# Kernel tuning notes

Measured on AMD Instinct MI355X. Metric: run time of the kernel, lower is better.

Reference implementation:

```python
import jax, jax.numpy as jnp
import numpy as np

B, T, C, H = 8, 2048, 1024, 128

def setup_inputs() -> dict:
    key = jax.random.key(0)
    k1, k2, k3, k4 = jax.random.split(key, 4)
    x = jax.random.normal(k1, (B, T, C), dtype=jnp.float32)
    Wq = jax.random.normal(k2, (C, H), dtype=jnp.float32) * (C ** -0.5)
    Wk = jax.random.normal(k3, (C, H), dtype=jnp.float32) * (C ** -0.5)
    Wv = jax.random.normal(k4, (C, H), dtype=jnp.float32) * (C ** -0.5)
    return {"x": x, "Wq": Wq, "Wk": Wk, "Wv": Wv}

def reference(x, Wq, Wk, Wv):
    # x: [B,T,C]; projections (no bias)
    q = jnp.einsum('btc,ch->bth', x, Wq)
    k = jnp.einsum('btc,ch->bth', x, Wk)
    v = jnp.einsum('btc,ch->bth', x, Wv)
    # NOTE: original module has NO 1/sqrt(head_size) scaling
    scores = jnp.einsum('bth,bsh->bts', q, k)  # [B,T,T]
    t = scores.shape[1]
    causal = jnp.tril(jnp.ones((t, t), dtype=bool))
    scores = jnp.where(causal, scores, -jnp.inf)
    attn = jax.nn.softmax(scores, axis=-1)  # dropout is identity in eval
    out = jnp.einsum('bts,bsh->bth', attn, v)  # [B,T,H]
    return out
```

## Files before the change

kernel.cpp:

```cpp
#include <hip/hip_runtime.h>

typedef __bf16 bf16;
typedef _Float16 f16;
typedef f16 f16x4 __attribute__((ext_vector_type(4)));
typedef f16 f16x8 __attribute__((ext_vector_type(8)));
typedef float f32x4 __attribute__((ext_vector_type(4)));

#define MFMA_FP(a, b, c) __builtin_amdgcn_mfma_f32_16x16x32_f16((a), (b), (c), 0, 0, 0)

static constexpr int Bn = 8, T = 2048, C = 1024, H = 128;
static constexpr int M = Bn * T;

__device__ __forceinline__ void gll16(const void* g, void* l) {
  __builtin_amdgcn_global_load_lds(
      (const __attribute__((address_space(1))) unsigned int*)g,
      (__attribute__((address_space(3))) unsigned int*)l, 16, 0, 0);
}

__global__ __launch_bounds__(256) void kwt(const float* __restrict__ Wq,
                                           const float* __restrict__ Wk,
                                           const float* __restrict__ Wv,
                                           f16* __restrict__ wt) {
  __shared__ float tl[32][33];
  const int w = blockIdx.z;
  const float* src = (w == 0) ? Wq : (w == 1) ? Wk : Wv;
  f16* dh = wt + (size_t)w * H * C;
  const int k0 = blockIdx.x * 32, n0 = blockIdx.y * 32;
  const int tx = threadIdx.x & 31, ty = threadIdx.x >> 5;
  for (int i = ty; i < 32; i += 8) tl[i][tx] = src[(size_t)(k0 + i) * H + n0 + tx];
  __syncthreads();
  for (int i = ty; i < 32; i += 8)
    dh[(size_t)(n0 + i) * C + k0 + tx] = (f16)tl[tx][i];
}

__global__ __launch_bounds__(256, 2) void proj_kernel(const float* __restrict__ x,
                                                      const f16* __restrict__ wt,
                                                      f16* __restrict__ qo,
                                                      f16* __restrict__ ko,
                                                      f16* __restrict__ vt) {
  __shared__ __align__(16) float As[2][64 * 64];
  __shared__ __align__(16) f16  Bs[2][128 * 64];
  const int tid = threadIdx.x;
  const int lane = tid & 63, g = lane >> 4, r16 = lane & 15;
  const int wave = tid >> 6, wr = wave >> 1, wc = wave & 1;
  const int m0 = blockIdx.x * 64;
  const int which = blockIdx.y;
  const f16* wh = wt + (size_t)which * H * C;

  int asrc[4], bsrc[4];
  int aldu[4], bldu[4];
#pragma unroll
  for (int i = 0; i < 4; ++i) {
    const int u = wave * 4 + i;
    const int ra = u * 4 + (lane >> 4);
    asrc[i] = (m0 + ra) * C + (((lane & 15) ^ (ra & 7)) << 2);
    aldu[i] = u * 256;
    const int rb = u * 8 + (lane >> 3);
    bsrc[i] = rb * C + (((lane & 7) ^ (rb & 7)) << 3);
    bldu[i] = u * 512;
  }

  f32x4 acc[2][4] = {};

#define ISSUE(K0, BUF)                                             \
  _Pragma("unroll")                                                \
  for (int i = 0; i < 4; ++i) {                                    \
    gll16(&x[asrc[i] + (K0)], &As[BUF][aldu[i]]);                  \
    gll16(&wh[bsrc[i] + (K0)], &Bs[BUF][bldu[i]]);                 \
  }

  ISSUE(0, 0);
  for (int k0 = 0; k0 < C; k0 += 64) {
    const int cur = (k0 >> 6) & 1;
    __syncthreads();
    if (k0 + 64 < C) ISSUE(k0 + 64, cur ^ 1);
#pragma unroll
    for (int kb = 0; kb < 2; ++kb) {
      f16x8 af[2], bf[4];
#pragma unroll
      for (int mt = 0; mt < 2; ++mt) {
        const int r = wr * 32 + mt * 16 + r16;
        const int s = r & 7;
        const f32x4 a0 = *(const f32x4*)&As[cur][r * 64 + (((kb * 8 + g * 2) ^ s) << 2)];
        const f32x4 a1 = *(const f32x4*)&As[cur][r * 64 + (((kb * 8 + g * 2 + 1) ^ s) << 2)];
#pragma unroll
        for (int j = 0; j < 4; ++j) { af[mt][j] = (f16)a0[j]; af[mt][4 + j] = (f16)a1[j]; }
      }
#pragma unroll
      for (int nt = 0; nt < 4; ++nt) {
        const int r = wc * 64 + nt * 16 + r16;
        const int phys = (kb * 4 + g) ^ (r & 7);
        bf[nt] = *(const f16x8*)&Bs[cur][r * 64 + phys * 8];
      }
#pragma unroll
      for (int mt = 0; mt < 2; ++mt)
#pragma unroll
        for (int nt = 0; nt < 4; ++nt)
          acc[mt][nt] = MFMA_FP(af[mt], bf[nt], acc[mt][nt]);
    }
  }
#undef ISSUE

  if (which < 2) {
    f16* dst = which ? ko : qo;
#pragma unroll
    for (int mt = 0; mt < 2; ++mt)
#pragma unroll
      for (int nt = 0; nt < 4; ++nt) {
        const int mb = m0 + wr * 32 + mt * 16 + g * 4;
        const int col = wc * 64 + nt * 16 + r16;
#pragma unroll
        for (int r = 0; r < 4; ++r)
          dst[(size_t)(mb + r) * H + col] = (f16)acc[mt][nt][r];
      }
  } else {
    const int b = m0 >> 11;
    const int tb0 = m0 & 2047;
    f16* vbase = vt + (size_t)b * H * T;
#pragma unroll
    for (int mt = 0; mt < 2; ++mt)
#pragma unroll
      for (int nt = 0; nt < 4; ++nt) {
        const int tib = tb0 + wr * 32 + mt * 16 + g * 4;
        const int h = wc * 64 + nt * 16 + r16;
        f16x4 pk;
#pragma unroll
        for (int r = 0; r < 4; ++r) pk[r] = (f16)acc[mt][nt][r];
        *(f16x4*)&vbase[(size_t)h * T + tib] = pk;
      }
  }
}

__global__ __launch_bounds__(256, 2) void attn_kernel(const f16* __restrict__ qp,
                                                      const f16* __restrict__ kp,
                                                      const f16* __restrict__ vp,
                                                      float* __restrict__ out,
                                                      f16* __restrict__ oS,
                                                      float* __restrict__ MLs) {
  __shared__ __align__(16) f16 KS[2][64 * 128];
  __shared__ __align__(16) f16 VS[2][128 * 64];
  __shared__ __align__(16) f16 Pl[4][16][72];

  const int tid = threadIdx.x, lane = tid & 63, wave = tid >> 6;
  const int g = lane >> 4, q15 = lane & 15;
  const int x7 = q15 & 7;
  const int bb = blockIdx.x;
  const int b = bb & 7;
  const int t2 = bb >> 3;
  const int qt = 31 - (t2 >> 1);
  const int par = t2 & 1;
  const int q0 = qt * 64;
  const int qrow = q0 + wave * 16 + q15;
  const int task = b * 32 + qt;

  const f16* qb = qp + (size_t)b * T * H;
  const f16* kb = kp + (size_t)b * T * H;
  const f16* vb = vp + (size_t)b * H * T;

  int koff[4], voff[4], lo[4];
#pragma unroll
  for (int i = 0; i < 4; ++i) {
    const int u = wave * 4 + i;
    const int rK = u * 4 + (lane >> 4);
    koff[i] = rK * H + (((lane & 15) ^ (rK & 7)) << 3);
    const int hV = u * 8 + (lane >> 3);
    voff[i] = hV * T + (((lane & 7) ^ (hV & 7)) << 3);
    lo[i] = u * 512 + lane * 8;
  }

  const int n = (qt >= par) ? ((qt - par) >> 1) + 1 : 0;

  f16x8 qf[4];
#pragma unroll
  for (int k4 = 0; k4 < 4; ++k4)
    qf[k4] = *(const f16x8*)&qb[(size_t)qrow * H + k4 * 32 + g * 8];

  f32x4 o[8] = {};
  float mrun = -1e30f, lrun = 0.f;

  f16x8 rk[4], rv[4];
#define LOADT(S0)                                                   \
  _Pragma("unroll")                                                 \
  for (int i = 0; i < 4; ++i) {                                     \
    rk[i] = *(const f16x8*)&kb[(size_t)(S0) * H + koff[i]];         \
    rv[i] = *(const f16x8*)&vb[(size_t)(S0) + voff[i]];             \
  }
#define WRITET(BUF)                                                 \
  _Pragma("unroll")                                                 \
  for (int i = 0; i < 4; ++i) {                                     \
    *(f16x8*)&KS[BUF][lo[i]] = rk[i];                               \
    *(f16x8*)&VS[BUF][lo[i]] = rv[i];                               \
  }

  if (n > 0) {
    LOADT(par * 64);
    WRITET(0);
    if (n > 1) LOADT(par * 64 + 128);

    for (int k = 0; k < n; ++k) {
      const int s0 = par * 64 + k * 128;
      const int cur = k & 1;
      __syncthreads();

      f32x4 sacc[4] = {};
#pragma unroll
      for (int mt = 0; mt < 4; ++mt) {
        const int row = mt * 16 + q15;
#pragma unroll
        for (int k4 = 0; k4 < 4; ++k4) {
          const int pch = (k4 * 4 + g) ^ (row & 7);
          const f16x8 kf = *(const f16x8*)&KS[cur][row * 128 + pch * 8];
          sacc[mt] = MFMA_FP(kf, qf[k4], sacc[mt]);
        }
      }
      if (k == n - 1) {
#pragma unroll
        for (int mt = 0; mt < 4; ++mt)
#pragma unroll
          for (int r = 0; r < 4; ++r)
            if (s0 + mt * 16 + g * 4 + r > qrow) sacc[mt][r] = -1e30f;
      }
      float tmax = -1e30f;
#pragma unroll
      for (int mt = 0; mt < 4; ++mt)
#pragma unroll
        for (int r = 0; r < 4; ++r) tmax = fmaxf(tmax, sacc[mt][r]);
      tmax = fmaxf(tmax, __shfl_xor(tmax, 16));
      tmax = fmaxf(tmax, __shfl_xor(tmax, 32));
      const float mnew = fmaxf(mrun, tmax);
      const float alpha = __expf(mrun - mnew);
      float lt = 0.f;
#pragma unroll
      for (int mt = 0; mt < 4; ++mt) {
        f16x4 pk;
#pragma unroll
        for (int r = 0; r < 4; ++r) {
          const float p = __expf(sacc[mt][r] - mnew);
          lt += p;
          pk[r] = (f16)p;
        }
        *(f16x4*)&Pl[wave][q15][mt * 16 + g * 4] = pk;
      }
      lt += __shfl_xor(lt, 16);
      lt += __shfl_xor(lt, 32);
      lrun = lrun * alpha + lt;
      mrun = mnew;
#pragma unroll
      for (int i = 0; i < 8; ++i) o[i] *= alpha;
      const f16x8 pf0 = *(const f16x8*)&Pl[wave][q15][g * 8];
      const f16x8 pf1 = *(const f16x8*)&Pl[wave][q15][32 + g * 8];
#pragma unroll
      for (int mt = 0; mt < 8; ++mt) {
        const int h = mt * 16 + q15;
        const f16x8 vf0 = *(const f16x8*)&VS[cur][h * 64 + ((g ^ x7) << 3)];
        o[mt] = MFMA_FP(vf0, pf0, o[mt]);
        const f16x8 vf1 = *(const f16x8*)&VS[cur][h * 64 + (((4 + g) ^ x7) << 3)];
        o[mt] = MFMA_FP(vf1, pf1, o[mt]);
      }

      if (k + 1 < n) {
        WRITET(cur ^ 1);
        if (k + 2 < n) LOADT(par * 64 + (k + 2) * 128);
      }
    }
  }
#undef LOADT
#undef WRITET

  const float inv = (lrun > 0.f) ? 1.0f / lrun : 0.f;
  if (lane < 16) {
    MLs[((size_t)(task * 2 + par) * 64 + wave * 16 + lane) * 2 + 0] = mrun;
    MLs[((size_t)(task * 2 + par) * 64 + wave * 16 + lane) * 2 + 1] = lrun;
  }
  if (par == 0) {
    float* ob = out + ((size_t)b * T + qrow) * H;
#pragma unroll
    for (int mt = 0; mt < 8; ++mt) {
      f32x4 pk;
#pragma unroll
      for (int r = 0; r < 4; ++r) pk[r] = o[mt][r] * inv;
      *(f32x4*)&ob[mt * 16 + g * 4] = pk;
    }
  } else {
    f16* sb = oS + ((size_t)task * 64 + wave * 16 + q15) * 128;
#pragma unroll
    for (int mt = 0; mt < 8; ++mt) {
      f16x4 pk;
#pragma unroll
      for (int r = 0; r < 4; ++r) pk[r] = (f16)(o[mt][r] * inv);
      *(f16x4*)&sb[mt * 16 + g * 4] = pk;
    }
  }
}

__global__ __launch_bounds__(256) void combine_kernel(float* __restrict__ out,
                                                      const f16* __restrict__ oS,
                                                      const float* __restrict__ MLs) {
  const int task = blockIdx.x;
  const int b = task >> 5, qt = task & 31;
  const int tid = threadIdx.x;
  const int row = tid >> 2;
  const int cb = (tid & 3) * 32;
  const float m0 = MLs[((size_t)(task * 2 + 0) * 64 + row) * 2 + 0];
  const float l0 = MLs[((size_t)(task * 2 + 0) * 64 + row) * 2 + 1];
  const float m1 = MLs[((size_t)(task * 2 + 1) * 64 + row) * 2 + 0];
  const float l1 = MLs[((size_t)(task * 2 + 1) * 64 + row) * 2 + 1];
  const float Mg = fmaxf(m0, m1);
  const float w0 = l0 * __expf(m0 - Mg);
  const float w1 = l1 * __expf(m1 - Mg);
  const float inv = 1.0f / (w0 + w1);
  float* orow = out + ((size_t)b * T + qt * 64 + row) * H + cb;
  const f16* srow = oS + ((size_t)task * 64 + row) * 128 + cb;
#pragma unroll
  for (int c = 0; c < 32; c += 8) {
    const f16x8 o1 = *(const f16x8*)&srow[c];
    f32x4 a0 = *(const f32x4*)&orow[c];
    f32x4 a1 = *(const f32x4*)&orow[c + 4];
    f32x4 r0, r1;
#pragma unroll
    for (int r = 0; r < 4; ++r) {
      r0[r] = (w0 * a0[r] + w1 * (float)o1[r]) * inv;
      r1[r] = (w0 * a1[r] + w1 * (float)o1[4 + r]) * inv;
    }
    *(f32x4*)&orow[c] = r0;
    *(f32x4*)&orow[c + 4] = r1;
  }
}

extern "C" void kernel_launch(void* const* d_in, const int* in_sizes, int n_in,
                              void* d_out, int out_size, void* d_ws, size_t ws_size,
                              hipStream_t stream) {
  const float* x  = (const float*)d_in[0];
  const float* Wq = (const float*)d_in[1];
  const float* Wk = (const float*)d_in[2];
  const float* Wv = (const float*)d_in[3];
  float* out = (float*)d_out;

  f16*  wt  = (f16*)d_ws;
  f16*  qf  = wt + (size_t)3 * H * C;
  f16*  kf  = qf + (size_t)M * H;
  f16*  vf  = kf + (size_t)M * H;
  f16*  oS  = vf + (size_t)M * H;
  float* MLs = (float*)(oS + (size_t)256 * 64 * 128);

  kwt<<<dim3(C / 32, H / 32, 3), 256, 0, stream>>>(Wq, Wk, Wv, wt);
  proj_kernel<<<dim3(M / 64, 3), 256, 0, stream>>>(x, wt, qf, kf, vf);
  attn_kernel<<<512, 256, 0, stream>>>(qf, kf, vf, out, oS, MLs);
  combine_kernel<<<256, 256, 0, stream>>>(out, oS, MLs);
}
```

Baseline: 78.37 us.

## Fuse Q/K/V projections into one 64x384 tile per block, converting x once

The projection kernel now computes all three Q, K and V outputs in one block per 64 rows, so x is read from global memory once instead of three times. x is loaded into registers, converted to fp16 and stored to LDS, which removes the per-fragment fp32-to-fp16 conversion and halves the A tile's LDS footprint. The grid drops from 768 blocks to 256 with a larger per-wave accumulator (4x6 MFMA tiles) and launch bounds allow only one block per CU. This risks lower occupancy, higher register pressure and less latency hiding on a GPU with 256 CUs.

```diff
diff --git a/kernel.cpp b/kernel.cpp
--- a/kernel.cpp
+++ b/kernel.cpp
@@ -33,101 +33,123 @@
     dh[(size_t)(n0 + i) * C + k0 + tx] = (f16)tl[tx][i];
 }
 
-__global__ __launch_bounds__(256, 2) void proj_kernel(const float* __restrict__ x,
+__global__ __launch_bounds__(256, 1) void proj_kernel(const float* __restrict__ x,
                                                       const f16* __restrict__ wt,
                                                       f16* __restrict__ qo,
                                                       f16* __restrict__ ko,
                                                       f16* __restrict__ vt) {
-  __shared__ __align__(16) float As[2][64 * 64];
-  __shared__ __align__(16) f16  Bs[2][128 * 64];
+  __shared__ __align__(16) f16 As[2][64 * 64];
+  __shared__ __align__(16) f16 Bs[2][384 * 64];
   const int tid = threadIdx.x;
   const int lane = tid & 63, g = lane >> 4, r16 = lane & 15;
-  const int wave = tid >> 6, wr = wave >> 1, wc = wave & 1;
+  const int wave = tid >> 6;
   const int m0 = blockIdx.x * 64;
-  const int which = blockIdx.y;
-  const f16* wh = wt + (size_t)which * H * C;
-
-  int asrc[4], bsrc[4];
-  int aldu[4], bldu[4];
-#pragma unroll
-  for (int i = 0; i < 4; ++i) {
-    const int u = wave * 4 + i;
-    const int ra = u * 4 + (lane >> 4);
-    asrc[i] = (m0 + ra) * C + (((lane & 15) ^ (ra & 7)) << 2);
-    aldu[i] = u * 256;
+
+  int bsrc[12];
+#pragma unroll
+  for (int i = 0; i < 12; ++i) {
+    const int u = wave * 12 + i;
     const int rb = u * 8 + (lane >> 3);
     bsrc[i] = rb * C + (((lane & 7) ^ (rb & 7)) << 3);
-    bldu[i] = u * 512;
-  }
-
-  f32x4 acc[2][4] = {};
-
-#define ISSUE(K0, BUF)                                             \
-  _Pragma("unroll")                                                \
-  for (int i = 0; i < 4; ++i) {                                    \
-    gll16(&x[asrc[i] + (K0)], &As[BUF][aldu[i]]);                  \
-    gll16(&wh[bsrc[i] + (K0)], &Bs[BUF][bldu[i]]);                 \
-  }
-
-  ISSUE(0, 0);
-  for (int k0 = 0; k0 < C; k0 += 64) {
-    const int cur = (k0 >> 6) & 1;
+  }
+  int asrc[2], aldw[2];
+#pragma unroll
+  for (int i = 0; i < 2; ++i) {
+    const int u = wave * 2 + i;
+    const int rA = u * 8 + (lane >> 3);
+    asrc[i] = (m0 + rA) * C + (((lane & 7) ^ (rA & 7)) << 3);
+    aldw[i] = rA * 64 + (lane & 7) * 8;
+  }
+
+  f32x4 acc[4][6] = {};
+  f32x4 arg[2][2];
+
+#define LOADA(K0)                                                   \
+  _Pragma("unroll")                                                 \
+  for (int i = 0; i < 2; ++i) {                                     \
+    arg[i][0] = *(const f32x4*)&x[asrc[i] + (K0)];                  \
+    arg[i][1] = *(const f32x4*)&x[asrc[i] + (K0) + 4];              \
+  }
+#define ISSUEB(K0, BUF)                                             \
+  _Pragma("unroll")                                                 \
+  for (int i = 0; i < 12; ++i)                                      \
+    gll16(&wt[bsrc[i] + (K0)], &Bs[BUF][(wave * 12 + i) * 512]);
+#define WRITEA(BUF)                                                 \
+  _Pragma("unroll")                                                 \
+  for (int i = 0; i < 2; ++i) {                                     \
+    f16x8 av;                                                       \
+    _Pragma("unroll")                                               \
+    for (int j = 0; j < 4; ++j) {                                   \
+      av[j] = (f16)arg[i][0][j];                                    \
+      av[4 + j] = (f16)arg[i][1][j];                                \
+    }                                                               \
+    *(f16x8*)&As[BUF][aldw[i]] = av;                                \
+  }
+
+  LOADA(0);
+  ISSUEB(0, 0);
+  WRITEA(0);
+
+  for (int k = 0; k < 16; ++k) {
+    const int cur = k & 1;
+    const int k0 = k * 64;
     __syncthreads();
-    if (k0 + 64 < C) ISSUE(k0 + 64, cur ^ 1);
+    if (k < 15) {
+      LOADA(k0 + 64);
+      ISSUEB(k0 + 64, cur ^ 1);
+    }
 #pragma unroll
     for (int kb = 0; kb < 2; ++kb) {
-      f16x8 af[2], bf[4];
-#pragma unroll
-      for (int mt = 0; mt < 2; ++mt) {
-        const int r = wr * 32 + mt * 16 + r16;
-        const int s = r & 7;
-        const f32x4 a0 = *(const f32x4*)&As[cur][r * 64 + (((kb * 8 + g * 2) ^ s) << 2)];
-        const f32x4 a1 = *(const f32x4*)&As[cur][r * 64 + (((kb * 8 + g * 2 + 1) ^ s) << 2)];
-#pragma unroll
-        for (int j = 0; j < 4; ++j) { af[mt][j] = (f16)a0[j]; af[mt][4 + j] = (f16)a1[j]; }
-      }
-#pragma unroll
-      for (int nt = 0; nt < 4; ++nt) {
-        const int r = wc * 64 + nt * 16 + r16;
+      f16x8 af[4], bf[6];
+#pragma unroll
+      for (int mt = 0; mt < 4; ++mt) {
+        const int r = mt * 16 + r16;
+        const int phys = (kb * 4 + g) ^ (r & 7);
+        af[mt] = *(const f16x8*)&As[cur][r * 64 + phys * 8];
+      }
+#pragma unroll
+      for (int nt = 0; nt < 6; ++nt) {
+        const int r = wave * 96 + nt * 16 + r16;
         const int phys = (kb * 4 + g) ^ (r & 7);
         bf[nt] = *(const f16x8*)&Bs[cur][r * 64 + phys * 8];
       }
 #pragma unroll
-      for (int mt = 0; mt < 2; ++mt)
-#pragma unroll
-        for (int nt = 0; nt < 4; ++nt)
+      for (int mt = 0; mt < 4; ++mt)
+#pragma unroll
+        for (int nt = 0; nt < 6; ++nt)
           acc[mt][nt] = MFMA_FP(af[mt], bf[nt], acc[mt][nt]);
     }
-  }
-#undef ISSUE
-
-  if (which < 2) {
-    f16* dst = which ? ko : qo;
-#pragma unroll
-    for (int mt = 0; mt < 2; ++mt)
-#pragma unroll
-      for (int nt = 0; nt < 4; ++nt) {
-        const int mb = m0 + wr * 32 + mt * 16 + g * 4;
-        const int col = wc * 64 + nt * 16 + r16;
+    if (k < 15) WRITEA(cur ^ 1);
+  }
+#undef LOADA
+#undef ISSUEB
+#undef WRITEA
+
+  const int b = m0 >> 11;
+  const int tb0 = m0 & 2047;
+  f16* vbase = vt + (size_t)b * H * T;
+#pragma unroll
+  for (int nt = 0; nt < 6; ++nt) {
+    const int nbase = wave * 96 + nt * 16;
+    const int which = nbase >> 7;
+#pragma unroll
+    for (int mt = 0; mt < 4; ++mt) {
+      if (which < 2) {
+        f16* dst = which ? ko : qo;
+        const int mb = m0 + mt * 16 + g * 4;
+        const int col = (nbase & 127) + r16;
 #pragma unroll
         for (int r = 0; r < 4; ++r)
           dst[(size_t)(mb + r) * H + col] = (f16)acc[mt][nt][r];
-      }
-  } else {
-    const int b = m0 >> 11;
-    const int tb0 = m0 & 2047;
-    f16* vbase = vt + (size_t)b * H * T;
-#pragma unroll
-    for (int mt = 0; mt < 2; ++mt)
-#pragma unroll
-      for (int nt = 0; nt < 4; ++nt) {
-        const int tib = tb0 + wr * 32 + mt * 16 + g * 4;
-        const int h = wc * 64 + nt * 16 + r16;
+      } else {
+        const int h = (nbase & 127) + r16;
+        const int tib = tb0 + mt * 16 + g * 4;
         f16x4 pk;
 #pragma unroll
         for (int r = 0; r < 4; ++r) pk[r] = (f16)acc[mt][nt][r];
         *(f16x4*)&vbase[(size_t)h * T + tib] = pk;
       }
+    }
   }
 }
 
@@ -344,7 +366,7 @@
   float* MLs = (float*)(oS + (size_t)256 * 64 * 128);
 
   kwt<<<dim3(C / 32, H / 32, 3), 256, 0, stream>>>(Wq, Wk, Wv, wt);
-  proj_kernel<<<dim3(M / 64, 3), 256, 0, stream>>>(x, wt, qf, kf, vf);
+  proj_kernel<<<256, 256, 0, stream>>>(x, wt, qf, kf, vf);
   attn_kernel<<<512, 256, 0, stream>>>(qf, kf, vf, out, oS, MLs);
   combine_kernel<<<256, 256, 0, stream>>>(out, oS, MLs);
 }
```

Result: slower. 80.65 us (+2.9%).

## Load projection operands directly from global into registers, dropping LDS staging

Applied to the files above, without the earlier changes.

The projection GEMM no longer stages x and weight tiles through double-buffered LDS with async global-to-LDS loads and block barriers. Each wave now loads its MFMA fragments straight from global memory into registers, with a one-step register prefetch, and occupancy is raised to three blocks per SM. This removes barriers and LDS traffic, but each fragment load is now a strided 16- or 32-byte access per lane. Operands shared across waves in a block are no longer reused through LDS, so global and cache traffic rise.

```diff
diff --git a/kernel.cpp b/kernel.cpp
--- a/kernel.cpp
+++ b/kernel.cpp
@@ -10,12 +10,6 @@
 
 static constexpr int Bn = 8, T = 2048, C = 1024, H = 128;
 static constexpr int M = Bn * T;
-
-__device__ __forceinline__ void gll16(const void* g, void* l) {
-  __builtin_amdgcn_global_load_lds(
-      (const __attribute__((address_space(1))) unsigned int*)g,
-      (__attribute__((address_space(3))) unsigned int*)l, 16, 0, 0);
-}
 
 __global__ __launch_bounds__(256) void kwt(const float* __restrict__ Wq,
                                            const float* __restrict__ Wk,
@@ -33,76 +27,69 @@
     dh[(size_t)(n0 + i) * C + k0 + tx] = (f16)tl[tx][i];
 }
 
-__global__ __launch_bounds__(256, 2) void proj_kernel(const float* __restrict__ x,
+__global__ __launch_bounds__(256, 3) void proj_kernel(const float* __restrict__ x,
                                                       const f16* __restrict__ wt,
                                                       f16* __restrict__ qo,
                                                       f16* __restrict__ ko,
                                                       f16* __restrict__ vt) {
-  __shared__ __align__(16) float As[2][64 * 64];
-  __shared__ __align__(16) f16  Bs[2][128 * 64];
   const int tid = threadIdx.x;
   const int lane = tid & 63, g = lane >> 4, r16 = lane & 15;
   const int wave = tid >> 6, wr = wave >> 1, wc = wave & 1;
   const int m0 = blockIdx.x * 64;
-  const int which = blockIdx.y;
-  const f16* wh = wt + (size_t)which * H * C;
-
-  int asrc[4], bsrc[4];
-  int aldu[4], bldu[4];
-#pragma unroll
-  for (int i = 0; i < 4; ++i) {
-    const int u = wave * 4 + i;
-    const int ra = u * 4 + (lane >> 4);
-    asrc[i] = (m0 + ra) * C + (((lane & 15) ^ (ra & 7)) << 2);
-    aldu[i] = u * 256;
-    const int rb = u * 8 + (lane >> 3);
-    bsrc[i] = rb * C + (((lane & 7) ^ (rb & 7)) << 3);
-    bldu[i] = u * 512;
-  }
+  const int nh = blockIdx.y;
+
+  const float* xr[2];
+  const f16* wrow[4];
+#pragma unroll
+  for (int mt = 0; mt < 2; ++mt)
+    xr[mt] = x + (size_t)(m0 + wr * 32 + mt * 16 + r16) * C + g * 8;
+#pragma unroll
+  for (int nt = 0; nt < 4; ++nt)
+    wrow[nt] = wt + (size_t)(nh * 128 + wc * 64 + nt * 16 + r16) * C + g * 8;
 
   f32x4 acc[2][4] = {};
 
-#define ISSUE(K0, BUF)                                             \
-  _Pragma("unroll")                                                \
-  for (int i = 0; i < 4; ++i) {                                    \
-    gll16(&x[asrc[i] + (K0)], &As[BUF][aldu[i]]);                  \
-    gll16(&wh[bsrc[i] + (K0)], &Bs[BUF][bldu[i]]);                 \
-  }
-
-  ISSUE(0, 0);
-  for (int k0 = 0; k0 < C; k0 += 64) {
-    const int cur = (k0 >> 6) & 1;
-    __syncthreads();
-    if (k0 + 64 < C) ISSUE(k0 + 64, cur ^ 1);
-#pragma unroll
-    for (int kb = 0; kb < 2; ++kb) {
-      f16x8 af[2], bf[4];
+  f32x4 a0[2], a1[2], a0n[2], a1n[2];
+  f16x8 bc[4], bn[4];
+#pragma unroll
+  for (int mt = 0; mt < 2; ++mt) {
+    a0[mt] = *(const f32x4*)(xr[mt]);
+    a1[mt] = *(const f32x4*)(xr[mt] + 4);
+  }
+#pragma unroll
+  for (int nt = 0; nt < 4; ++nt) bc[nt] = *(const f16x8*)(wrow[nt]);
+
+  for (int k = 0; k < C; k += 32) {
+    if (k + 32 < C) {
 #pragma unroll
       for (int mt = 0; mt < 2; ++mt) {
-        const int r = wr * 32 + mt * 16 + r16;
-        const int s = r & 7;
-        const f32x4 a0 = *(const f32x4*)&As[cur][r * 64 + (((kb * 8 + g * 2) ^ s) << 2)];
-        const f32x4 a1 = *(const f32x4*)&As[cur][r * 64 + (((kb * 8 + g * 2 + 1) ^ s) << 2)];
-#pragma unroll
-        for (int j = 0; j < 4; ++j) { af[mt][j] = (f16)a0[j]; af[mt][4 + j] = (f16)a1[j]; }
-      }
-#pragma unroll
-      for (int nt = 0; nt < 4; ++nt) {
-        const int r = wc * 64 + nt * 16 + r16;
-        const int phys = (kb * 4 + g) ^ (r & 7);
-        bf[nt] = *(const f16x8*)&Bs[cur][r * 64 + phys * 8];
-      }
-#pragma unroll
-      for (int mt = 0; mt < 2; ++mt)
-#pragma unroll
-        for (int nt = 0; nt < 4; ++nt)
-          acc[mt][nt] = MFMA_FP(af[mt], bf[nt], acc[mt][nt]);
-    }
-  }
-#undef ISSUE
-
-  if (which < 2) {
-    f16* dst = which ? ko : qo;
+        a0n[mt] = *(const f32x4*)(xr[mt] + k + 32);
+        a1n[mt] = *(const f32x4*)(xr[mt] + k + 36);
+      }
+#pragma unroll
+      for (int nt = 0; nt < 4; ++nt) bn[nt] = *(const f16x8*)(wrow[nt] + k + 32);
+    }
+    f16x8 af[2];
+#pragma unroll
+    for (int mt = 0; mt < 2; ++mt)
+#pragma unroll
+      for (int j = 0; j < 4; ++j) {
+        af[mt][j] = (f16)a0[mt][j];
+        af[mt][4 + j] = (f16)a1[mt][j];
+      }
+#pragma unroll
+    for (int mt = 0; mt < 2; ++mt)
+#pragma unroll
+      for (int nt = 0; nt < 4; ++nt)
+        acc[mt][nt] = MFMA_FP(af[mt], bc[nt], acc[mt][nt]);
+#pragma unroll
+    for (int mt = 0; mt < 2; ++mt) { a0[mt] = a0n[mt]; a1[mt] = a1n[mt]; }
+#pragma unroll
+    for (int nt = 0; nt < 4; ++nt) bc[nt] = bn[nt];
+  }
+
+  if (nh < 2) {
+    f16* dst = nh ? ko : qo;
 #pragma unroll
     for (int mt = 0; mt < 2; ++mt)
 #pragma unroll
```

New measurement: 128.9 us. +64.5%, slower.

## Stage x as fp16 in LDS via registers and skip softmax rescale lazily

Applied to the files above, without the earlier changes.

The projection kernel now loads x tiles into registers, converts them to fp16 and writes them to LDS. This replaces the direct fp32 global-to-LDS copies, halving the A-tile LDS footprint, and occupancy is raised to 3 blocks per SM. The attention kernel skips the running-max rescale of the output accumulator unless some lane's tile max exceeds the running max by more than 8. This trades exact online-softmax bookkeeping for fewer exponentials and multiplies, at the risk of fp16 P values up to e^8 losing headroom.

```diff
diff --git a/kernel.cpp b/kernel.cpp
--- a/kernel.cpp
+++ b/kernel.cpp
@@ -33,13 +33,13 @@
     dh[(size_t)(n0 + i) * C + k0 + tx] = (f16)tl[tx][i];
 }
 
-__global__ __launch_bounds__(256, 2) void proj_kernel(const float* __restrict__ x,
+__global__ __launch_bounds__(256, 3) void proj_kernel(const float* __restrict__ x,
                                                       const f16* __restrict__ wt,
                                                       f16* __restrict__ qo,
                                                       f16* __restrict__ ko,
                                                       f16* __restrict__ vt) {
-  __shared__ __align__(16) float As[2][64 * 64];
-  __shared__ __align__(16) f16  Bs[2][128 * 64];
+  __shared__ __align__(16) f16 As[2][64 * 64];
+  __shared__ __align__(16) f16 Bs[2][128 * 64];
   const int tid = threadIdx.x;
   const int lane = tid & 63, g = lane >> 4, r16 = lane & 15;
   const int wave = tid >> 6, wr = wave >> 1, wc = wave & 1;
@@ -47,44 +47,67 @@
   const int which = blockIdx.y;
   const f16* wh = wt + (size_t)which * H * C;
 
-  int asrc[4], bsrc[4];
-  int aldu[4], bldu[4];
+  int asrc[2], aldw[2], bsrc[4], bldu[4];
+#pragma unroll
+  for (int i = 0; i < 2; ++i) {
+    const int u = wave * 2 + i;
+    const int rA = u * 8 + (lane >> 3);
+    asrc[i] = (m0 + rA) * C + (((lane & 7) ^ (rA & 7)) << 3);
+    aldw[i] = rA * 64 + (lane & 7) * 8;
+  }
 #pragma unroll
   for (int i = 0; i < 4; ++i) {
     const int u = wave * 4 + i;
-    const int ra = u * 4 + (lane >> 4);
-    asrc[i] = (m0 + ra) * C + (((lane & 15) ^ (ra & 7)) << 2);
-    aldu[i] = u * 256;
     const int rb = u * 8 + (lane >> 3);
     bsrc[i] = rb * C + (((lane & 7) ^ (rb & 7)) << 3);
     bldu[i] = u * 512;
   }
 
   f32x4 acc[2][4] = {};
-
-#define ISSUE(K0, BUF)                                             \
+  f32x4 arg[2][2];
+
+#define LOADA(K0)                                                  \
   _Pragma("unroll")                                                \
-  for (int i = 0; i < 4; ++i) {                                    \
-    gll16(&x[asrc[i] + (K0)], &As[BUF][aldu[i]]);                  \
-    gll16(&wh[bsrc[i] + (K0)], &Bs[BUF][bldu[i]]);                 \
-  }
-
-  ISSUE(0, 0);
-  for (int k0 = 0; k0 < C; k0 += 64) {
-    const int cur = (k0 >> 6) & 1;
+  for (int i = 0; i < 2; ++i) {                                    \
+    arg[i][0] = *(const f32x4*)&x[asrc[i] + (K0)];                 \
+    arg[i][1] = *(const f32x4*)&x[asrc[i] + (K0) + 4];             \
+  }
+#define ISSUEB(K0, BUF)                                            \
+  _Pragma("unroll")                                                \
+  for (int i = 0; i < 4; ++i)                                      \
+    gll16(&wh[bsrc[i] + (K0)], &Bs[BUF][bldu[i]]);
+#define WRITEA(BUF)                                                \
+  _Pragma("unroll")                                                \
+  for (int i = 0; i < 2; ++i) {                                    \
+    f16x8 av;                                                      \
+    _Pragma("unroll")                                              \
+    for (int j = 0; j < 4; ++j) {                                  \
+      av[j] = (f16)arg[i][0][j];                                   \
+      av[4 + j] = (f16)arg[i][1][j];                               \
+    }                                                              \
+    *(f16x8*)&As[BUF][aldw[i]] = av;                               \
+  }
+
+  LOADA(0);
+  ISSUEB(0, 0);
+  WRITEA(0);
+
+  for (int k = 0; k < 16; ++k) {
+    const int cur = k & 1;
+    const int k0 = k * 64;
     __syncthreads();
-    if (k0 + 64 < C) ISSUE(k0 + 64, cur ^ 1);
+    if (k < 15) {
+      LOADA(k0 + 64);
+      ISSUEB(k0 + 64, cur ^ 1);
+    }
 #pragma unroll
     for (int kb = 0; kb < 2; ++kb) {
       f16x8 af[2], bf[4];
 #pragma unroll
       for (int mt = 0; mt < 2; ++mt) {
         const int r = wr * 32 + mt * 16 + r16;
-        const int s = r & 7;
-        const f32x4 a0 = *(const f32x4*)&As[cur][r * 64 + (((kb * 8 + g * 2) ^ s) << 2)];
-        const f32x4 a1 = *(const f32x4*)&As[cur][r * 64 + (((kb * 8 + g * 2 + 1) ^ s) << 2)];
-#pragma unroll
-        for (int j = 0; j < 4; ++j) { af[mt][j] = (f16)a0[j]; af[mt][4 + j] = (f16)a1[j]; }
+        const int phys = (kb * 4 + g) ^ (r & 7);
+        af[mt] = *(const f16x8*)&As[cur][r * 64 + phys * 8];
       }
 #pragma unroll
       for (int nt = 0; nt < 4; ++nt) {
@@ -98,8 +121,11 @@
         for (int nt = 0; nt < 4; ++nt)
           acc[mt][nt] = MFMA_FP(af[mt], bf[nt], acc[mt][nt]);
     }
-  }
-#undef ISSUE
+    if (k < 15) WRITEA(cur ^ 1);
+  }
+#undef LOADA
+#undef ISSUEB
+#undef WRITEA
 
   if (which < 2) {
     f16* dst = which ? ko : qo;
@@ -227,15 +253,21 @@
         for (int r = 0; r < 4; ++r) tmax = fmaxf(tmax, sacc[mt][r]);
       tmax = fmaxf(tmax, __shfl_xor(tmax, 16));
       tmax = fmaxf(tmax, __shfl_xor(tmax, 32));
-      const float mnew = fmaxf(mrun, tmax);
-      const float alpha = __expf(mrun - mnew);
+      if (!__all(tmax <= mrun + 8.f)) {
+        const float mnew = fmaxf(mrun, tmax);
+        const float alpha = __expf(mrun - mnew);
+        lrun *= alpha;
+#pragma unroll
+        for (int i = 0; i < 8; ++i) o[i] *= alpha;
+        mrun = mnew;
+      }
       float lt = 0.f;
 #pragma unroll
       for (int mt = 0; mt < 4; ++mt) {
         f16x4 pk;
 #pragma unroll
         for (int r = 0; r < 4; ++r) {
-          const float p = __expf(sacc[mt][r] - mnew);
+          const float p = __expf(sacc[mt][r] - mrun);
           lt += p;
           pk[r] = (f16)p;
         }
@@ -243,10 +275,7 @@
       }
       lt += __shfl_xor(lt, 16);
       lt += __shfl_xor(lt, 32);
-      lrun = lrun * alpha + lt;
-      mrun = mnew;
-#pragma unroll
-      for (int i = 0; i < 8; ++i) o[i] *= alpha;
+      lrun += lt;
       const f16x8 pf0 = *(const f16x8*)&Pl[wave][q15][g * 8];
       const f16x8 pf1 = *(const f16x8*)&Pl[wave][q15][32 + g * 8];
 #pragma unroll
```

Result: faster. 67.41 us (-14.0%).
